# Kernel optimization log

Measured on AMD Instinct MI355X. Metric: run time of the kernel, lower is better.

## Reference

```python
import jax, jax.numpy as jnp
import numpy as np
import math

# Module constants derived from init_kwargs
DIM1, DIM2 = 32, 32          # n_patches = (512//16, 512//16)
PREFIX = 8                   # num_prefix_tokens
STD = 5.0                    # gauss_std
NUM_HEADS = 12               # orig_attn.num_heads (ViT-B)
EMBED_DIM = 768


def gaussian_window(n1, n2, std):
    # torch linspace(start*c, (start+(n-1))*c, n) == (arange(n)-(n-1)/2)*c
    c = 1.0 / (std * math.sqrt(2.0))
    k1 = (jnp.arange(n1, dtype=jnp.float32) - (n1 - 1) / 2.0) * c
    k2 = (jnp.arange(n2, dtype=jnp.float32) - (n2 - 1) / 2.0) * c
    return jnp.exp(-(k1[:, None] ** 2 + k2[None, :] ** 2))


def attn_addition():
    # Same-padding cross-correlation of per-token delta images with the window
    # collapses to: add[(i,l),(p,q)] = window[i-p+DIM1-1, l-q+DIM2-1]
    win = gaussian_window(2 * DIM1 - 1, 2 * DIM2 - 1, STD)
    i = jnp.arange(DIM1)
    l = jnp.arange(DIM2)
    di = i[:, None] - i[None, :] + (DIM1 - 1)   # [i, p]
    dl = l[:, None] - l[None, :] + (DIM2 - 1)   # [l, q]
    add = win[di[:, None, :, None], dl[None, :, None, :]]  # [i, l, p, q]
    add = add.reshape(DIM1 * DIM2, DIM1 * DIM2)
    # zero rows/cols for prefix tokens (prepended)
    return jnp.pad(add, ((PREFIX, 0), (PREFIX, 0)))


def setup_inputs() -> dict:
    key = jax.random.key(0)
    ks = jax.random.split(key, 5)
    B, N, C = 8, DIM1 * DIM2 + PREFIX, EMBED_DIM
    return {
        "x": jax.random.normal(ks[0], (B, N, C), dtype=jnp.float32),
        "qkv_w": jax.random.normal(ks[1], (3 * C, C), dtype=jnp.float32) * 0.02,
        "qkv_b": jax.random.normal(ks[2], (3 * C,), dtype=jnp.float32) * 0.02,
        "proj_w": jax.random.normal(ks[3], (C, C), dtype=jnp.float32) * 0.02,
        "proj_b": jax.random.normal(ks[4], (C,), dtype=jnp.float32) * 0.02,
    }


def reference(x, qkv_w, qkv_b, proj_w, proj_b):
    B, N, C = x.shape
    H = NUM_HEADS
    hd = C // H
    scale = hd ** (-0.5)
    add = attn_addition()  # [N, N] constant bias

    qkv = x @ qkv_w.T + qkv_b                      # [B, N, 3C]
    q, k, v = jnp.split(qkv, 3, axis=-1)           # q computed but unused (k.k^T attention)
    k = k.reshape(B, N, H, hd)
    v = v.reshape(B, N, H, hd)

    attn = jnp.einsum("bihd,bjhd->bhij", k, k) * scale + add[None, None]
    attn = jax.nn.softmax(attn, axis=-1)
    out = jnp.einsum("bhij,bjhd->bihd", attn, v).reshape(B, N, C)
    out = out @ proj_w.T + proj_b
    return out
```

## Files before the change

### kernel.cpp

```cpp
#include <hip/hip_runtime.h>
#include <stdint.h>

typedef __bf16 bf16;
typedef _Float16 f16;
typedef __bf16 bf16x8 __attribute__((ext_vector_type(8)));
typedef __bf16 bf16x4 __attribute__((ext_vector_type(4)));
typedef float f32x4 __attribute__((ext_vector_type(4)));

#define NSEQ 1032
#define BATCH 8
#define NHEADS 12
#define HD 64
#define CDIM 768
#define MROWS (BATCH * NSEQ)
#define PREFIX 8
#define NJT 17
#define NQ16 72
#define KSTRIDE 1152
#define VSTRIDE 1152
#define KSCALE 0.42466090f

__device__ __forceinline__ unsigned short f2bf_rne(float f) {
    union { float f; uint32_t u; } v; v.f = f;
    uint32_t u = v.u;
    return (unsigned short)((u + 0x7fffu + ((u >> 16) & 1u)) >> 16);
}

__device__ __forceinline__ void gload_lds16(const bf16* g, bf16* l) {
    __builtin_amdgcn_global_load_lds(
        (const __attribute__((address_space(1))) void*)g,
        (__attribute__((address_space(3))) void*)l, 16, 0, 0);
}

__device__ __forceinline__ void cast4(const float* src, bf16* dst, int i) {
    float4 f = ((const float4*)src)[i];
    ushort4 o;
    o.x = f2bf_rne(f.x); o.y = f2bf_rne(f.y);
    o.z = f2bf_rne(f.z); o.w = f2bf_rne(f.w);
    ((ushort4*)dst)[i] = o;
}

__device__ __forceinline__ void bar() {
    asm volatile("s_waitcnt lgkmcnt(0)" ::: "memory");
    __builtin_amdgcn_s_barrier();
    asm volatile("" ::: "memory");
}

__device__ __forceinline__ void gbar() {
    asm volatile("s_waitcnt vmcnt(0)" ::: "memory");
    __builtin_amdgcn_s_barrier();
    asm volatile("" ::: "memory");
}

__global__ void prep_kernel(const float* __restrict__ x,
                            const float* __restrict__ wkv,
                            const float* __restrict__ pw,
                            bf16* __restrict__ x_bf, bf16* __restrict__ wkv_bf,
                            bf16* __restrict__ pw_bf, float* __restrict__ Bias,
                            bf16* __restrict__ k_bf, bf16* __restrict__ vt_bf) {
    const int N0 = NQ16 * NJT * 1024;
    const int N1 = MROWS * CDIM / 4;
    const int N2 = 2 * CDIM * CDIM / 4;
    const int N3 = CDIM * CDIM / 4;
    const int N4 = BATCH * NHEADS * 120 * 8;
    const int N5 = BATCH * NHEADS * 64 * 15;
    int i = blockIdx.x * blockDim.x + threadIdx.x;
    if (i < N0) {
        int r    = i & 3;
        int l15  = (i >> 2) & 15;
        int quad = (i >> 6) & 3;
        int kt   = (i >> 8) & 3;
        int rest = i >> 10;
        int q16  = rest / NJT;
        int jt   = rest - q16 * NJT;
        int q = q16 * 16 + l15;
        int k = jt * 64 + kt * 16 + quad * 4 + r;
        float v;
        if (k >= NSEQ) v = -65504.f;
        else if (q < PREFIX || q >= NSEQ || k < PREFIX) v = 0.f;
        else {
            int rp = q - PREFIX, cp = k - PREFIX;
            int d1 = (rp >> 5) - (cp >> 5);
            int d2 = (rp & 31) - (cp & 31);
            v = 1.44269504f * __expf(-0.02f * (float)(d1 * d1 + d2 * d2));
        }
        Bias[i] = v;
        return;
    }
    i -= N0;
    if (i < N1) { cast4(x, x_bf, i); return; }
    i -= N1;
    if (i < N2) { cast4(wkv, wkv_bf, i); return; }
    i -= N2;
    if (i < N3) { cast4(pw, pw_bf, i); return; }
    i -= N3;
    if (i < N4) {
        int bh = i / 960, rem = i - bh * 960;
        int row = 1032 + (rem >> 3), ch = rem & 7;
        uint4 z = {0u, 0u, 0u, 0u};
        *(uint4*)&k_bf[((size_t)bh * KSTRIDE + row) * HD + ch * 8] = z;
        return;
    }
    i -= N4;
    if (i < N5) {
        int bh = i / 960, rem = i - bh * 960;
        int d = rem / 15, ch = rem - d * 15;
        uint4 z = {0u, 0u, 0u, 0u};
        *(uint4*)&vt_bf[((size_t)bh * HD + d) * VSTRIDE + 1032 + ch * 8] = z;
    }
}

template<int EPI>
__global__ __launch_bounds__(256) void gemm_nt(
    const bf16* __restrict__ A, const bf16* __restrict__ B,
    const float* __restrict__ bias,
    float* __restrict__ Cout, bf16* __restrict__ Kout, bf16* __restrict__ Vout,
    int M, int N, int K)
{
    __shared__ bf16 sA[2][128 * 32];
    __shared__ bf16 sB[2][128 * 32];
    const int t = threadIdx.x;
    const int w = t >> 6;
    const int l = t & 63;
    const int quad = l >> 4;
    const int l15 = l & 15;
    const int wy = w >> 1, wx = w & 1;
    const int m0 = blockIdx.y * 128;
    const int n0 = blockIdx.x * 128;
    const int co = (quad ^ ((l15 >> 1) & 3)) * 8;

    int r0 = t >> 2,          c0 = (t & 3) ^ ((r0 >> 1) & 3);
    int r1 = (t + 256) >> 2,  c1 = ((t + 256) & 3) ^ ((r1 >> 1) & 3);
    int ra0 = m0 + r0; if (ra0 >= M) ra0 = M - 1;
    int ra1 = m0 + r1; if (ra1 >= M) ra1 = M - 1;
    const bf16* gA0 = A + (size_t)ra0 * K + c0 * 8;
    const bf16* gA1 = A + (size_t)ra1 * K + c1 * 8;
    const bf16* gB0 = B + (size_t)(n0 + r0) * K + c0 * 8;
    const bf16* gB1 = B + (size_t)(n0 + r1) * K + c1 * 8;
    const int oA0 = (w * 64) * 8;
    const int oA1 = (256 + w * 64) * 8;

    f32x4 acc[4][4] = {};

#define STAGE(BUF) do { \
        gload_lds16(gA0, &sA[BUF][oA0]); gload_lds16(gA1, &sA[BUF][oA1]); \
        gload_lds16(gB0, &sB[BUF][oA0]); gload_lds16(gB1, &sB[BUF][oA1]); \
        gA0 += 32; gA1 += 32; gB0 += 32; gB1 += 32; \
    } while (0)

#define COMPUTE(BUF) do { \
        bf16x8 af_[4], bq_[4]; \
        _Pragma("unroll") \
        for (int mt = 0; mt < 4; ++mt) \
            af_[mt] = *(const bf16x8*)&sA[BUF][(wy*64 + mt*16 + l15) * 32 + co]; \
        _Pragma("unroll") \
        for (int nt = 0; nt < 4; ++nt) \
            bq_[nt] = *(const bf16x8*)&sB[BUF][(wx*64 + nt*16 + l15) * 32 + co]; \
        _Pragma("unroll") \
        for (int mt = 0; mt < 4; ++mt) \
            _Pragma("unroll") \
            for (int nt = 0; nt < 4; ++nt) \
                acc[mt][nt] = __builtin_amdgcn_mfma_f32_16x16x32_bf16( \
                    af_[mt], bq_[nt], acc[mt][nt], 0, 0, 0); \
    } while (0)

    STAGE(0);
    gbar();
    const int NP = K / 64;
    #pragma unroll 1
    for (int p = 0; p < NP; ++p) {
        STAGE(1);
        COMPUTE(0);
        gbar();
        if (p + 1 < NP) STAGE(0);
        COMPUTE(1);
        gbar();
    }
#undef STAGE
#undef COMPUTE

    if (EPI == 0) {
        #pragma unroll
        for (int mt = 0; mt < 4; ++mt) {
            #pragma unroll
            for (int r = 0; r < 4; ++r) {
                int m = m0 + wy*64 + mt*16 + quad*4 + r;
                if (m >= M) continue;
                #pragma unroll
                for (int nt = 0; nt < 4; ++nt) {
                    int n = n0 + wx*64 + nt*16 + l15;
                    Cout[(size_t)m * N + n] = acc[mt][nt][r] + bias[n];
                }
            }
        }
    } else {
        #pragma unroll
        for (int mt = 0; mt < 4; ++mt) {
            int mb = m0 + wy*64 + mt*16 + quad*4;
            if (mb >= M) continue;
            int b = mb / NSEQ, s = mb % NSEQ;
            #pragma unroll
            for (int nt = 0; nt < 4; ++nt) {
                int n = n0 + wx*64 + nt*16 + l15;
                float bn = bias[n];
                if (n < CDIM) {
                    int h = n >> 6, d = n & 63;
                    bf16* kp = &Kout[(((size_t)(b*NHEADS + h))*KSTRIDE + s)*HD + d];
                    #pragma unroll
                    for (int r = 0; r < 4; ++r)
                        kp[(size_t)r * HD] = (bf16)((acc[mt][nt][r] + bn) * KSCALE);
                } else {
                    int n2 = n - CDIM;
                    int h = n2 >> 6, d = n2 & 63;
                    bf16x4 pv = { (bf16)(acc[mt][nt][0] + bn), (bf16)(acc[mt][nt][1] + bn),
                                  (bf16)(acc[mt][nt][2] + bn), (bf16)(acc[mt][nt][3] + bn) };
                    *(bf16x4*)&Vout[(((size_t)(b*NHEADS + h))*HD + d)*VSTRIDE + s] = pv;
                }
            }
        }
    }
}

__global__ __launch_bounds__(256) void attn_kernel(
    const bf16* __restrict__ Kbuf, const bf16* __restrict__ VTbuf,
    const float* __restrict__ Bias, bf16* __restrict__ Hout)
{
    const int bh = blockIdx.x;
    const int b = bh / NHEADS, h = bh % NHEADS;
    const int q0 = blockIdx.y * 128;
    const bf16* Kh  = Kbuf  + (size_t)bh * KSTRIDE * HD;
    const bf16* VTh = VTbuf + (size_t)bh * HD * VSTRIDE;

    __shared__ bf16 sK[2][64 * 64];
    __shared__ bf16 sVT[2][64 * 64];
    __shared__ bf16 sP[128 * 64];

    const int t = threadIdx.x;
    const int w = t >> 6, l = t & 63, quad = l >> 4, l15 = l & 15;
    const int sw = l15 & 7;

    const int r0 = t >> 3, c0 = t & 7;
    const int r1 = r0 + 32;
    const int dk0 = r0*64 + ((c0 ^ (r0 & 7)) << 3);
    const int dk1 = r1*64 + ((c0 ^ (r1 & 7)) << 3);

    const bf16* pK0 = Kh + (size_t)r0 * HD + c0 * 8;
    const bf16* pK1 = Kh + (size_t)r1 * HD + c0 * 8;
    const bf16* pV0 = VTh + (size_t)r0 * VSTRIDE + c0 * 8;
    const bf16* pV1 = VTh + (size_t)r1 * VSTRIDE + c0 * 8;
    const float* pB0 = Bias + ((size_t)(blockIdx.y*8 + w*2 + 0) * NJT) * 1024 + quad*64 + l15*4;
    const float* pB1 = Bias + ((size_t)(blockIdx.y*8 + w*2 + 1) * NJT) * 1024 + quad*64 + l15*4;

    bf16x8 qf[2][2];
    #pragma unroll
    for (int qh = 0; qh < 2; ++qh) {
        int row = q0 + w*32 + qh*16 + l15;
        #pragma unroll
        for (int ks = 0; ks < 2; ++ks)
            qf[qh][ks] = *(const bf16x8*)&Kh[(size_t)row * HD + ks*32 + quad*8];
    }

    bf16x8 onesb;
    #pragma unroll
    for (int e = 0; e < 8; ++e) onesb[e] = (bf16)1.0f;

    f32x4 Oacc[2][4] = {};
    f32x4 Lacc[2] = {};
    const int sPr0 = (w*32 + l15) * 64;

    uint4 kva, kvb, vva, vvb;
    f32x4 bpA[2][4], bpB[2][4];

#define PREFETCH_KV() do { \
        kva = *(const uint4*)pK0; kvb = *(const uint4*)pK1; \
        vva = *(const uint4*)pV0; vvb = *(const uint4*)pV1; \
        pK0 += 64*HD; pK1 += 64*HD; pV0 += 64; pV1 += 64; \
    } while (0)

#define PREFETCH_B(BANK) do { \
        _Pragma("unroll") \
        for (int kt = 0; kt < 4; ++kt) { \
            BANK[0][kt] = *(const f32x4*)(pB0 + kt*256); \
            BANK[1][kt] = *(const f32x4*)(pB1 + kt*256); \
        } \
        pB0 += 1024; pB1 += 1024; \
    } while (0)

#define ITER(CUR, ACC, NEXT) do { \
        *(uint4*)&sK[CUR][dk0] = kva; *(uint4*)&sK[CUR][dk1] = kvb; \
        *(uint4*)&sVT[CUR][dk0] = vva; *(uint4*)&sVT[CUR][dk1] = vvb; \
        PREFETCH_KV(); \
        PREFETCH_B(NEXT); \
        bar(); \
        _Pragma("unroll") \
        for (int ks = 0; ks < 2; ++ks) { \
            bf16x8 af[4]; \
            _Pragma("unroll") \
            for (int kt = 0; kt < 4; ++kt) \
                af[kt] = *(const bf16x8*)&sK[CUR][(kt*16 + l15)*64 + (((ks*4 + quad) ^ sw) << 3)]; \
            __builtin_amdgcn_s_setprio(1); \
            _Pragma("unroll") \
            for (int qh = 0; qh < 2; ++qh) \
                _Pragma("unroll") \
                for (int kt = 0; kt < 4; ++kt) \
                    ACC[qh][kt] = __builtin_amdgcn_mfma_f32_16x16x32_bf16( \
                        af[kt], qf[qh][ks], ACC[qh][kt], 0, 0, 0); \
            __builtin_amdgcn_s_setprio(0); \
        } \
        _Pragma("unroll") \
        for (int qh = 0; qh < 2; ++qh) \
            _Pragma("unroll") \
            for (int kt = 0; kt < 4; ++kt) { \
                float p0 = __builtin_exp2f(ACC[qh][kt][0]); \
                float p1 = __builtin_exp2f(ACC[qh][kt][1]); \
                float p2 = __builtin_exp2f(ACC[qh][kt][2]); \
                float p3 = __builtin_exp2f(ACC[qh][kt][3]); \
                bf16x4 pv = { (bf16)p0, (bf16)p1, (bf16)p2, (bf16)p3 }; \
                int g = (kt*2 + (quad >> 1)) ^ sw; \
                *(bf16x4*)&sP[sPr0 + qh*1024 + g*8 + (quad & 1)*4] = pv; \
            } \
        _Pragma("unroll") \
        for (int ks = 0; ks < 2; ++ks) { \
            bf16x8 bv[4]; \
            _Pragma("unroll") \
            for (int dt = 0; dt < 4; ++dt) \
                bv[dt] = *(const bf16x8*)&sVT[CUR][(dt*16 + l15)*64 + (((ks*4 + quad) ^ sw) << 3)]; \
            __builtin_amdgcn_s_setprio(1); \
            _Pragma("unroll") \
            for (int qh = 0; qh < 2; ++qh) { \
                bf16x8 ap = *(const bf16x8*)&sP[sPr0 + qh*1024 + (((ks*4 + quad) ^ sw) * 8)]; \
                _Pragma("unroll") \
                for (int dt = 0; dt < 4; ++dt) \
                    Oacc[qh][dt] = __builtin_amdgcn_mfma_f32_16x16x32_bf16( \
                        ap, bv[dt], Oacc[qh][dt], 0, 0, 0); \
                Lacc[qh] = __builtin_amdgcn_mfma_f32_16x16x32_bf16( \
                    ap, onesb, Lacc[qh], 0, 0, 0); \
            } \
            __builtin_amdgcn_s_setprio(0); \
        } \
    } while (0)

    PREFETCH_KV();
    PREFETCH_B(bpA);
    ITER(0, bpA, bpB);
    #pragma unroll 1
    for (int it = 0; it < (NJT - 1) / 2; ++it) {
        ITER(1, bpB, bpA);
        ITER(0, bpA, bpB);
    }
#undef ITER
#undef PREFETCH_KV
#undef PREFETCH_B

    #pragma unroll
    for (int qh = 0; qh < 2; ++qh)
        #pragma unroll
        for (int r = 0; r < 4; ++r) {
            int g = q0 + w*32 + qh*16 + quad*4 + r;
            if (g >= NSEQ) continue;
            float inv = 1.f / Lacc[qh][r];
            size_t base = ((size_t)(b * NSEQ) + g) * CDIM + h * HD;
            #pragma unroll
            for (int dt = 0; dt < 4; ++dt)
                Hout[base + dt*16 + l15] = (bf16)(Oacc[qh][dt][r] * inv);
        }
}

extern "C" void kernel_launch(void* const* d_in, const int* in_sizes, int n_in,
                              void* d_out, int out_size, void* d_ws, size_t ws_size,
                              hipStream_t stream) {
    const float* x      = (const float*)d_in[0];
    const float* qkv_w  = (const float*)d_in[1];
    const float* qkv_b  = (const float*)d_in[2];
    const float* proj_w = (const float*)d_in[3];
    const float* proj_b = (const float*)d_in[4];
    float* out = (float*)d_out;

    char* ws = (char*)d_ws;
    const size_t XBF_BYTES   = (size_t)MROWS * CDIM * 2;
    const size_t WKV_BYTES   = (size_t)2 * CDIM * CDIM * 2;
    const size_t PW_BYTES    = (size_t)CDIM * CDIM * 2;
    const size_t BIAS_BYTES  = (size_t)NQ16 * NJT * 1024 * 4;
    const size_t KBF_BYTES   = (size_t)BATCH * NHEADS * KSTRIDE * HD * 2;

    bf16*  x_bf   = (bf16*)ws;
    bf16*  wkv_bf = (bf16*)(ws + XBF_BYTES);
    bf16*  pw_bf  = (bf16*)(ws + XBF_BYTES + WKV_BYTES);
    float* bias_t = (float*)(ws + XBF_BYTES + WKV_BYTES + PW_BYTES);
    bf16*  k_bf   = (bf16*)(ws + XBF_BYTES + WKV_BYTES + PW_BYTES + BIAS_BYTES);
    bf16*  vt_bf  = (bf16*)(ws + XBF_BYTES + WKV_BYTES + PW_BYTES + BIAS_BYTES + KBF_BYTES);

    {
        int total = NQ16 * NJT * 1024 + MROWS * CDIM / 4
                  + 2 * CDIM * CDIM / 4 + CDIM * CDIM / 4
                  + BATCH * NHEADS * 120 * 8 + BATCH * NHEADS * 64 * 15;
        prep_kernel<<<dim3((total + 255) / 256), dim3(256), 0, stream>>>(
            x, qkv_w + (size_t)CDIM * CDIM, proj_w, x_bf, wkv_bf, pw_bf, bias_t,
            k_bf, vt_bf);
    }

    {
        dim3 grid(1536 / 128, (MROWS + 127) / 128);
        gemm_nt<1><<<grid, dim3(256), 0, stream>>>(x_bf, wkv_bf, qkv_b + CDIM,
                                                   nullptr, k_bf, vt_bf,
                                                   MROWS, 1536, CDIM);
    }

    {
        dim3 grid(BATCH * NHEADS, (NSEQ + 127) / 128);
        attn_kernel<<<grid, dim3(256), 0, stream>>>(k_bf, vt_bf, bias_t, x_bf);
    }

    {
        dim3 grid(CDIM / 128, (MROWS + 127) / 128);
        gemm_nt<0><<<grid, dim3(256), 0, stream>>>(x_bf, pw_bf, proj_b,
                                                   out, nullptr, nullptr,
                                                   MROWS, CDIM, CDIM);
    }
}
```

Baseline: 225.6 us.

## Halve attention query tile to 64 rows and add XCD-aware GEMM block remap

```diff
diff --git a/kernel.cpp b/kernel.cpp
--- a/kernel.cpp
+++ b/kernel.cpp
@@ -125,8 +125,18 @@
     const int quad = l >> 4;
     const int l15 = l & 15;
     const int wy = w >> 1, wx = w & 1;
-    const int m0 = blockIdx.y * 128;
-    const int n0 = blockIdx.x * 128;
+
+    const int nbx = gridDim.x;
+    int id = blockIdx.y * nbx + blockIdx.x;
+    {
+        int nwg = nbx * gridDim.y;
+        int qq = nwg >> 3, rr = nwg & 7;
+        int xcd = id & 7, idx = id >> 3;
+        id = (xcd < rr) ? (xcd * (qq + 1) + idx)
+                        : (rr * (qq + 1) + (xcd - rr) * qq + idx);
+    }
+    const int m0 = (id / nbx) * 128;
+    const int n0 = (id % nbx) * 128;
     const int co = (quad ^ ((l15 >> 1) & 3)) * 8;
 
     int r0 = t >> 2,          c0 = (t & 3) ^ ((r0 >> 1) & 3);
@@ -227,13 +237,13 @@
 {
     const int bh = blockIdx.x;
     const int b = bh / NHEADS, h = bh % NHEADS;
-    const int q0 = blockIdx.y * 128;
+    const int q0 = blockIdx.y * 64;
     const bf16* Kh  = Kbuf  + (size_t)bh * KSTRIDE * HD;
     const bf16* VTh = VTbuf + (size_t)bh * HD * VSTRIDE;
 
     __shared__ bf16 sK[2][64 * 64];
     __shared__ bf16 sVT[2][64 * 64];
-    __shared__ bf16 sP[128 * 64];
+    __shared__ bf16 sP[64 * 64];
 
     const int t = threadIdx.x;
     const int w = t >> 6, l = t & 63, quad = l >> 4, l15 = l & 15;
@@ -248,28 +258,26 @@
     const bf16* pK1 = Kh + (size_t)r1 * HD + c0 * 8;
     const bf16* pV0 = VTh + (size_t)r0 * VSTRIDE + c0 * 8;
     const bf16* pV1 = VTh + (size_t)r1 * VSTRIDE + c0 * 8;
-    const float* pB0 = Bias + ((size_t)(blockIdx.y*8 + w*2 + 0) * NJT) * 1024 + quad*64 + l15*4;
-    const float* pB1 = Bias + ((size_t)(blockIdx.y*8 + w*2 + 1) * NJT) * 1024 + quad*64 + l15*4;
-
-    bf16x8 qf[2][2];
-    #pragma unroll
-    for (int qh = 0; qh < 2; ++qh) {
-        int row = q0 + w*32 + qh*16 + l15;
+    const float* pB = Bias + (size_t)(blockIdx.y*4 + w) * NJT * 1024 + quad*64 + l15*4;
+
+    bf16x8 qf[2];
+    {
+        int row = q0 + w*16 + l15;
         #pragma unroll
         for (int ks = 0; ks < 2; ++ks)
-            qf[qh][ks] = *(const bf16x8*)&Kh[(size_t)row * HD + ks*32 + quad*8];
+            qf[ks] = *(const bf16x8*)&Kh[(size_t)row * HD + ks*32 + quad*8];
     }
 
     bf16x8 onesb;
     #pragma unroll
     for (int e = 0; e < 8; ++e) onesb[e] = (bf16)1.0f;
 
-    f32x4 Oacc[2][4] = {};
-    f32x4 Lacc[2] = {};
-    const int sPr0 = (w*32 + l15) * 64;
+    f32x4 Oacc[4] = {};
+    f32x4 Lacc = {};
+    const int sPr0 = (w*16 + l15) * 64;
 
     uint4 kva, kvb, vva, vvb;
-    f32x4 bpA[2][4], bpB[2][4];
+    f32x4 bpA[4], bpB[4];
 
 #define PREFETCH_KV() do { \
         kva = *(const uint4*)pK0; kvb = *(const uint4*)pK1; \
@@ -279,11 +287,9 @@
 
 #define PREFETCH_B(BANK) do { \
         _Pragma("unroll") \
-        for (int kt = 0; kt < 4; ++kt) { \
-            BANK[0][kt] = *(const f32x4*)(pB0 + kt*256); \
-            BANK[1][kt] = *(const f32x4*)(pB1 + kt*256); \
-        } \
-        pB0 += 1024; pB1 += 1024; \
+        for (int kt = 0; kt < 4; ++kt) \
+            BANK[kt] = *(const f32x4*)(pB + kt*256); \
+        pB += 1024; \
     } while (0)
 
 #define ITER(CUR, ACC, NEXT) do { \
@@ -300,25 +306,21 @@
                 af[kt] = *(const bf16x8*)&sK[CUR][(kt*16 + l15)*64 + (((ks*4 + quad) ^ sw) << 3)]; \
             __builtin_amdgcn_s_setprio(1); \
             _Pragma("unroll") \
-            for (int qh = 0; qh < 2; ++qh) \
-                _Pragma("unroll") \
-                for (int kt = 0; kt < 4; ++kt) \
-                    ACC[qh][kt] = __builtin_amdgcn_mfma_f32_16x16x32_bf16( \
-                        af[kt], qf[qh][ks], ACC[qh][kt], 0, 0, 0); \
+            for (int kt = 0; kt < 4; ++kt) \
+                ACC[kt] = __builtin_amdgcn_mfma_f32_16x16x32_bf16( \
+                    af[kt], qf[ks], ACC[kt], 0, 0, 0); \
             __builtin_amdgcn_s_setprio(0); \
         } \
         _Pragma("unroll") \
-        for (int qh = 0; qh < 2; ++qh) \
-            _Pragma("unroll") \
-            for (int kt = 0; kt < 4; ++kt) { \
-                float p0 = __builtin_exp2f(ACC[qh][kt][0]); \
-                float p1 = __builtin_exp2f(ACC[qh][kt][1]); \
-                float p2 = __builtin_exp2f(ACC[qh][kt][2]); \
-                float p3 = __builtin_exp2f(ACC[qh][kt][3]); \
-                bf16x4 pv = { (bf16)p0, (bf16)p1, (bf16)p2, (bf16)p3 }; \
-                int g = (kt*2 + (quad >> 1)) ^ sw; \
-                *(bf16x4*)&sP[sPr0 + qh*1024 + g*8 + (quad & 1)*4] = pv; \
-            } \
+        for (int kt = 0; kt < 4; ++kt) { \
+            float p0 = __builtin_exp2f(ACC[kt][0]); \
+            float p1 = __builtin_exp2f(ACC[kt][1]); \
+            float p2 = __builtin_exp2f(ACC[kt][2]); \
+            float p3 = __builtin_exp2f(ACC[kt][3]); \
+            bf16x4 pv = { (bf16)p0, (bf16)p1, (bf16)p2, (bf16)p3 }; \
+            int g = (kt*2 + (quad >> 1)) ^ sw; \
+            *(bf16x4*)&sP[sPr0 + g*8 + (quad & 1)*4] = pv; \
+        } \
         _Pragma("unroll") \
         for (int ks = 0; ks < 2; ++ks) { \
             bf16x8 bv[4]; \
@@ -326,16 +328,13 @@
             for (int dt = 0; dt < 4; ++dt) \
                 bv[dt] = *(const bf16x8*)&sVT[CUR][(dt*16 + l15)*64 + (((ks*4 + quad) ^ sw) << 3)]; \
             __builtin_amdgcn_s_setprio(1); \
+            bf16x8 ap = *(const bf16x8*)&sP[sPr0 + (((ks*4 + quad) ^ sw) * 8)]; \
             _Pragma("unroll") \
-            for (int qh = 0; qh < 2; ++qh) { \
-                bf16x8 ap = *(const bf16x8*)&sP[sPr0 + qh*1024 + (((ks*4 + quad) ^ sw) * 8)]; \
-                _Pragma("unroll") \
-                for (int dt = 0; dt < 4; ++dt) \
-                    Oacc[qh][dt] = __builtin_amdgcn_mfma_f32_16x16x32_bf16( \
-                        ap, bv[dt], Oacc[qh][dt], 0, 0, 0); \
-                Lacc[qh] = __builtin_amdgcn_mfma_f32_16x16x32_bf16( \
-                    ap, onesb, Lacc[qh], 0, 0, 0); \
-            } \
+            for (int dt = 0; dt < 4; ++dt) \
+                Oacc[dt] = __builtin_amdgcn_mfma_f32_16x16x32_bf16( \
+                    ap, bv[dt], Oacc[dt], 0, 0, 0); \
+            Lacc = __builtin_amdgcn_mfma_f32_16x16x32_bf16( \
+                ap, onesb, Lacc, 0, 0, 0); \
             __builtin_amdgcn_s_setprio(0); \
         } \
     } while (0)
@@ -353,17 +352,15 @@
 #undef PREFETCH_B
 
     #pragma unroll
-    for (int qh = 0; qh < 2; ++qh)
+    for (int r = 0; r < 4; ++r) {
+        int g = q0 + w*16 + quad*4 + r;
+        if (g >= NSEQ) continue;
+        float inv = 1.f / Lacc[r];
+        size_t base = ((size_t)(b * NSEQ) + g) * CDIM + h * HD;
         #pragma unroll
-        for (int r = 0; r < 4; ++r) {
-            int g = q0 + w*32 + qh*16 + quad*4 + r;
-            if (g >= NSEQ) continue;
-            float inv = 1.f / Lacc[qh][r];
-            size_t base = ((size_t)(b * NSEQ) + g) * CDIM + h * HD;
-            #pragma unroll
-            for (int dt = 0; dt < 4; ++dt)
-                Hout[base + dt*16 + l15] = (bf16)(Oacc[qh][dt][r] * inv);
-        }
+        for (int dt = 0; dt < 4; ++dt)
+            Hout[base + dt*16 + l15] = (bf16)(Oacc[dt][r] * inv);
+    }
 }
 
 extern "C" void kernel_launch(void* const* d_in, const int* in_sizes, int n_in,
@@ -407,7 +404,7 @@
     }
 
     {
-        dim3 grid(BATCH * NHEADS, (NSEQ + 127) / 128);
+        dim3 grid(BATCH * NHEADS, 17);
         attn_kernel<<<grid, dim3(256), 0, stream>>>(k_bf, vt_bf, bias_t, x_bf);
     }
 
```

Result: no change. 226.4 us (+0.3%).
